# Kernel tuning notes

Measured on AMD Instinct MI355X. Metric: run time of the kernel, lower is better.

The kernel has to match this reference:

```python
import jax, jax.numpy as jnp
import numpy as np

# ---- constants mirroring the module config ----
NH = 64          # num_horizontal
NV = 8           # num_vertical (height slices)
GH = 51.2        # grid_size_h (meters)
GV = 8.0         # grid_size_v (meters)
HF, WF = 26, 88  # ground feature map spatial shape (grd_spatial_shape_cross)
IMG_H, IMG_W = 416.0, 1408.0  # kitti_grd_size (H, W)
C = 256          # embed_dim
HEADS = 8
P = 4            # num_points (num_levels = 1)
DH = C // HEADS
NU = NH // 2 + 1  # 33
LQ = NU * NH      # 2112 queries


def _grid3d():
    x_ = np.linspace(-GH / 2, 0, NU)
    y_ = np.linspace(-GH / 2, GH / 2, NH)
    z_ = np.linspace(-GV / 2, GV / 2, NV)
    gx, gy, gz = np.meshgrid(x_, y_, z_, indexing='ij')
    g = np.stack([gy, -gz, -gx], axis=-1).reshape(-1, 3).astype(np.float32)
    return jnp.asarray(g)  # (NU*NH*NV, 3)


def setup_inputs() -> dict:
    key = jax.random.key(0)
    ks = jax.random.split(key, 8)
    bs = 2
    query = jax.random.normal(ks[0], (bs, LQ, C), jnp.float32)
    value = jax.random.normal(ks[1], (bs, HF * WF, C), jnp.float32)
    K = jnp.array([[984.0, 0.0, 704.0], [0.0, 984.0, 208.0], [0.0, 0.0, 1.0]], jnp.float32)
    camera_k = jnp.broadcast_to(K, (bs, 3, 3))
    s = 1.0 / np.sqrt(C)
    Wv = jax.random.normal(ks[2], (C, C), jnp.float32) * s
    bv = jnp.zeros((C,), jnp.float32)
    Wo = jax.random.normal(ks[3], (C, HEADS * P * 2), jnp.float32) * 0.02
    bo = jax.random.normal(ks[4], (HEADS * P * 2,), jnp.float32) * 0.5
    Wa = jax.random.normal(ks[5], (C, HEADS * P), jnp.float32) * 0.02
    ba = jnp.zeros((HEADS * P,), jnp.float32)
    Wout = jax.random.normal(ks[6], (C, C), jnp.float32) * s
    bout = jnp.zeros((C,), jnp.float32)
    Wp = jax.random.normal(ks[7], (C, 1), jnp.float32) * s
    bp = jnp.zeros((1,), jnp.float32)
    return dict(query=query, value=value, camera_k=camera_k, Wv=Wv, bv=bv,
                Wo=Wo, bo=bo, Wa=Wa, ba=ba, Wout=Wout, bout=bout, Wp=Wp, bp=bp)


def _bilinear(val, x, y):
    # val: (bs, HF, WF, heads, dh); x, y: (bs, S, heads) pixel coords (align_corners=False, zero pad)
    bs, H_, W_, nh, _ = val.shape
    x0f = jnp.floor(x)
    y0f = jnp.floor(y)
    lx = x - x0f
    ly = y - y0f
    x0 = x0f.astype(jnp.int32)
    y0 = y0f.astype(jnp.int32)
    b_idx = jnp.arange(bs)[:, None, None]
    h_idx = jnp.arange(nh)[None, None, :]

    def corner(xi, yi, w):
        valid = (xi >= 0) & (xi < W_) & (yi >= 0) & (yi < H_)
        xc = jnp.clip(xi, 0, W_ - 1)
        yc = jnp.clip(yi, 0, H_ - 1)
        g = val[b_idx, yc, xc, h_idx]  # (bs, S, heads, dh)
        return g * (w * valid)[..., None]

    return (corner(x0, y0, (1 - lx) * (1 - ly))
            + corner(x0 + 1, y0, lx * (1 - ly))
            + corner(x0, y0 + 1, (1 - lx) * ly)
            + corner(x0 + 1, y0 + 1, lx * ly))


def reference(query, value, camera_k, Wv, bv, Wo, bo, Wa, ba, Wout, bout, Wp, bp):
    bs = query.shape[0]
    g = _grid3d()                                       # (N3, 3)
    proj = jnp.einsum('bij,nj->bin', camera_k, g)       # (bs, 3, N3)
    den = proj[:, 2]
    den = jnp.where(jnp.abs(den) < 1e-6, 1e-6, den)     # sanitize depth-0 points
    u = (proj[:, 0] / den / IMG_W).reshape(bs, NU, NH, NV)
    v = (proj[:, 1] / den / IMG_H).reshape(bs, NU, NH, NV)
    keep_index = ((u >= 0) & (u <= 1) & (v >= 0) & (v <= 1)).sum(-1).astype(bool)

    # --- MultiScaleDeformableAttention, vectorized over the NV height slices ---
    valp = (value @ Wv + bv).reshape(bs, HF, WF, HEADS, DH)
    off = (query @ Wo + bo).reshape(bs, LQ, HEADS, P, 2)
    attn = jax.nn.softmax((query @ Wa + ba).reshape(bs, LQ, HEADS, P), axis=-1)

    ref = jnp.stack([u, v], axis=-1).transpose(0, 3, 1, 2, 4).reshape(bs, NV, LQ, 2)
    norm = jnp.array([WF, HF], jnp.float32)            # offset_normalizer = (W, H)
    loc = ref[:, :, :, None, None, :] + off[:, None] / norm  # (bs, NV, LQ, heads, P, 2)
    # grid_sample align_corners=False: pixel = loc*size - 0.5
    px = jnp.clip(loc[..., 0] * WF - 0.5, -1e4, 1e4)
    py = jnp.clip(loc[..., 1] * HF - 0.5, -1e4, 1e4)
    px = px.transpose(0, 1, 2, 4, 3).reshape(bs, -1, HEADS)  # (bs, NV*LQ*P, heads)
    py = py.transpose(0, 1, 2, 4, 3).reshape(bs, -1, HEADS)
    sampled = _bilinear(valp, px, py).reshape(bs, NV, LQ, P, HEADS, DH)
    msda = jnp.einsum('bqhp,bvqphd->bvqhd', attn, sampled).reshape(bs, NV, LQ, C)
    grd_bev_v = msda @ Wout + bout + query[:, None]     # MSDA internal identity residual

    # --- softmax-weighted pooling over height ---
    grd_3d = grd_bev_v.reshape(bs, NV, NU, NH, C).transpose(0, 2, 3, 1, 4)  # (bs,NU,NH,NV,C)
    w = jax.nn.softmax(grd_3d @ Wp + bp, axis=3)        # (bs, NU, NH, NV, 1)
    max_height_index = jnp.argmax(w, axis=3)            # (bs, NU, NH, 1)
    grd_bev = (w * grd_3d).sum(3).reshape(bs, LQ, C) + query
    return grd_bev, max_height_index, keep_index
```

## Files before the change

### kernel.cpp

```cpp
#include <hip/hip_runtime.h>
#include <hip/hip_bf16.h>

constexpr int kNV = 8;
constexpr int kHF = 26;
constexpr int kWF = 88;
constexpr int kC  = 256;
constexpr int kP  = 4;
constexpr int kNU = 33;
constexpr int kNH = 64;
constexpr int kLQ = kNU * kNH;

typedef short short8 __attribute__((ext_vector_type(8)));
typedef float floatx4 __attribute__((ext_vector_type(4)));

__device__ __forceinline__ unsigned short f2bf(float x) {
  __hip_bfloat16 h = __float2bfloat16(x);
  unsigned short u;
  __builtin_memcpy(&u, &h, 2);
  return u;
}

template <bool VIRT>
__device__ __forceinline__ void gemm_body(
    const float* __restrict__ A, const float* __restrict__ B,
    const float* __restrict__ bias,
    const float* __restrict__ Wo, const float* __restrict__ Wa,
    const float* __restrict__ bo, const float* __restrict__ ba,
    float* __restrict__ out, int M, int N, int K, int bx, int by) {
  __shared__ float As[32][36];
  __shared__ float Bs[32][64];
  int tid = threadIdx.x;
  int tx = tid & 15, ty = tid >> 4;
  int row0 = by * 32, col0 = bx * 64;
  int ar = tid >> 3, ak = (tid & 7) * 4;
  int bc = (tid & 15) * 4, bk = tid >> 4;
  bool arow_ok = (row0 + ar) < M;
  const float* Ap = A + (size_t)(row0 + ar) * K + ak;
  int cb = col0 + bc;
  float acc[2][4] = {};
  for (int k0 = 0; k0 < K; k0 += 32) {
    float4 a4 = {0.f, 0.f, 0.f, 0.f};
    if (arow_ok) a4 = *reinterpret_cast<const float4*>(Ap + k0);
    float4 b0, b1;
    if (!VIRT) {
      b0 = *reinterpret_cast<const float4*>(&B[(size_t)(k0 + bk) * N + cb]);
      b1 = *reinterpret_cast<const float4*>(&B[(size_t)(k0 + bk + 16) * N + cb]);
    } else {
      if (cb < 64) {
        b0 = *reinterpret_cast<const float4*>(&Wo[(k0 + bk) * 64 + cb]);
        b1 = *reinterpret_cast<const float4*>(&Wo[(k0 + bk + 16) * 64 + cb]);
      } else if (cb < 96) {
        b0 = *reinterpret_cast<const float4*>(&Wa[(k0 + bk) * 32 + cb - 64]);
        b1 = *reinterpret_cast<const float4*>(&Wa[(k0 + bk + 16) * 32 + cb - 64]);
      } else {
        b0 = float4{0.f, 0.f, 0.f, 0.f};
        b1 = float4{0.f, 0.f, 0.f, 0.f};
      }
    }
    __syncthreads();
    *reinterpret_cast<float4*>(&As[ar][ak]) = a4;
    *reinterpret_cast<float4*>(&Bs[bk][bc]) = b0;
    *reinterpret_cast<float4*>(&Bs[bk + 16][bc]) = b1;
    __syncthreads();
#pragma unroll
    for (int kk = 0; kk < 32; ++kk) {
      float a0 = As[ty * 2][kk];
      float a1 = As[ty * 2 + 1][kk];
      float4 b4 = *reinterpret_cast<const float4*>(&Bs[kk][tx * 4]);
      acc[0][0] += a0 * b4.x; acc[0][1] += a0 * b4.y;
      acc[0][2] += a0 * b4.z; acc[0][3] += a0 * b4.w;
      acc[1][0] += a1 * b4.x; acc[1][1] += a1 * b4.y;
      acc[1][2] += a1 * b4.z; acc[1][3] += a1 * b4.w;
    }
  }
  int gc = col0 + tx * 4;
  float4 bi;
  if (!VIRT) {
    bi = *reinterpret_cast<const float4*>(&bias[gc]);
  } else if (gc < 64) {
    bi = *reinterpret_cast<const float4*>(&bo[gc]);
  } else if (gc < 96) {
    bi = *reinterpret_cast<const float4*>(&ba[gc - 64]);
  } else {
    bi = float4{0.f, 0.f, 0.f, 0.f};
  }
#pragma unroll
  for (int i = 0; i < 2; ++i) {
    int gr = row0 + ty * 2 + i;
    if (gr >= M) continue;
    float4 r;
    r.x = acc[i][0] + bi.x; r.y = acc[i][1] + bi.y;
    r.z = acc[i][2] + bi.z; r.w = acc[i][3] + bi.w;
    *reinterpret_cast<float4*>(&out[(size_t)gr * N + gc]) = r;
  }
}

__global__ __launch_bounds__(256) void k_front(
    const float* __restrict__ value, const float* __restrict__ Wv,
    const float* __restrict__ bv, float* __restrict__ valp,
    const float* __restrict__ query, float* __restrict__ qcat,
    const float* __restrict__ Wo, const float* __restrict__ Wa,
    const float* __restrict__ bo, const float* __restrict__ ba,
    const float* __restrict__ camk, float* __restrict__ uv,
    float* __restrict__ out_keep,
    const float* __restrict__ Wout, const float* __restrict__ Wp,
    float* __restrict__ WoutWp, unsigned short* __restrict__ WoutT,
    int bs, int MV, int MQ, int nValp, int nQ, int nGeomBlk) {
  int blk = blockIdx.x;
  int tid = threadIdx.x;
  if (blk < nValp) {
    gemm_body<false>(value, Wv, bv, nullptr, nullptr, nullptr, nullptr,
                     valp, MV, kC, kC, blk & 3, blk >> 2);
  } else if (blk < nValp + nQ) {
    int r = blk - nValp;
    gemm_body<true>(query, nullptr, nullptr, Wo, Wa, bo, ba,
                    qcat, MQ, 128, kC, r & 1, r >> 1);
  } else if (blk < nValp + nQ + nGeomBlk) {
    int t = (blk - nValp - nQ) * 256 + tid;
    if (t >= bs * kLQ) return;
    int b = t / kLQ;
    int ij = t - b * kLQ;
    int i = ij / kNH;
    int j = ij - i * kNH;
    const float* K = camk + b * 9;
    float g0 = (float)(-25.6 + (double)j * (51.2 / 63.0));
    float g2 = (float)(25.6 - (double)i * 0.8);
    bool any = false;
    float* dst = uv + (size_t)t * 16;
    for (int k = 0; k < kNV; ++k) {
      float g1 = (float)(4.0 - (double)k * (8.0 / 7.0));
      float p0 = K[0] * g0 + K[1] * g1 + K[2] * g2;
      float p1 = K[3] * g0 + K[4] * g1 + K[5] * g2;
      float p2 = K[6] * g0 + K[7] * g1 + K[8] * g2;
      float den = (fabsf(p2) < 1e-6f) ? 1e-6f : p2;
      float u = p0 / den / 1408.0f;
      float v = p1 / den / 416.0f;
      any = any || (u >= 0.f && u <= 1.f && v >= 0.f && v <= 1.f);
      dst[k * 2]     = u;
      dst[k * 2 + 1] = v;
    }
    out_keep[t] = any ? 1.f : 0.f;
  } else if (blk < nValp + nQ + nGeomBlk + 64) {
    int r = (blk - nValp - nQ - nGeomBlk) * 4 + (tid >> 6);
    int lane = tid & 63;
    const float* row = Wout + (size_t)r * kC;
    float s = 0.f;
#pragma unroll
    for (int j = lane; j < kC; j += 64) s += row[j] * Wp[j];
#pragma unroll
    for (int o = 32; o > 0; o >>= 1) s += __shfl_down(s, o, 64);
    if (lane == 0) WoutWp[r] = s;
  } else {
    int c = blk - nValp - nQ - nGeomBlk - 64;
    WoutT[(size_t)c * kC + tid] = f2bf(Wout[(size_t)tid * kC + c]);
  }
}

__global__ __launch_bounds__(256) void gemm_mfma(
    const unsigned short* __restrict__ Abf, const unsigned short* __restrict__ BT,
    const float* __restrict__ bias, const float* __restrict__ query,
    float* __restrict__ out, int M) {
  int gw = blockIdx.x * 4 + (threadIdx.x >> 6);
  int lane = threadIdx.x & 63;
  int tr = gw >> 4;
  int tc = gw & 15;
  int r0 = tr * 16, c0 = tc * 16;
  if (r0 >= M) return;
  int lrow = lane & 15;
  int kgrp = lane >> 4;
  const unsigned short* Ap = Abf + (size_t)(r0 + lrow) * kC + kgrp * 8;
  const unsigned short* Bp = BT  + (size_t)(c0 + lrow) * kC + kgrp * 8;
  floatx4 acc = {0.f, 0.f, 0.f, 0.f};
#pragma unroll
  for (int k0 = 0; k0 < kC; k0 += 32) {
    short8 a = *reinterpret_cast<const short8*>(Ap + k0);
    short8 b = *reinterpret_cast<const short8*>(Bp + k0);
    acc = __builtin_amdgcn_mfma_f32_16x16x32_bf16(a, b, acc, 0, 0, 0);
  }
  int col = c0 + lrow;
  float bi = bias[col];
#pragma unroll
  for (int r = 0; r < 4; ++r) {
    int row = r0 + kgrp * 4 + r;
    out[(size_t)row * kC + col] =
        acc[r] + bi + 2.0f * query[(size_t)row * kC + col];
  }
}

__global__ __launch_bounds__(256) void k_fused(
    const float* __restrict__ valp, const float* __restrict__ uv,
    const float* __restrict__ qcat, const float* __restrict__ WoutWp,
    unsigned short* __restrict__ msda_bf, float* __restrict__ out_mhi) {
  int bq = blockIdx.x;
  int b = bq / kLQ;
  int tid = threadIdx.x;
  int wp = tid >> 6;
  int lane = tid & 63;
  int h = lane >> 3;
  int dq = lane & 7;
  int ch = h * 32 + dq * 4;

  const float* qp = qcat + (size_t)bq * 128;

  float4 qa4 = *reinterpret_cast<const float4*>(qp + 64 + h * 4);
  float am = fmaxf(fmaxf(qa4.x, qa4.y), fmaxf(qa4.z, qa4.w));
  float e0 = expf(qa4.x - am), e1 = expf(qa4.y - am);
  float e2 = expf(qa4.z - am), e3 = expf(qa4.w - am);
  float ei = 1.f / (e0 + e1 + e2 + e3);
  float aw[4] = {e0 * ei, e1 * ei, e2 * ei, e3 * ei};

  float4 qo0 = *reinterpret_cast<const float4*>(qp + h * 8);
  float4 qo1 = *reinterpret_cast<const float4*>(qp + h * 8 + 4);
  float offx[4] = {qo0.x, qo0.z, qo1.x, qo1.z};
  float offy[4] = {qo0.y, qo0.w, qo1.y, qo1.w};

  float4 t4 = reinterpret_cast<const float4*>(uv + (size_t)bq * 16)[wp];
  float ub[2], vb[2];
  ub[0] = t4.x * 88.0f - 0.5f;
  vb[0] = t4.y * 26.0f - 0.5f;
  ub[1] = t4.z * 88.0f - 0.5f;
  vb[1] = t4.w * 26.0f - 0.5f;

  const float* vp = valp + (size_t)b * (kHF * kWF) * kC + ch;
  float4 w4 = *reinterpret_cast<const float4*>(WoutWp + ch);

  __shared__ float lgs[kNV];
  __shared__ float wks[kNV];
  __shared__ float4 part[3][64];

  float4 sv[2];
#pragma unroll
  for (int vv = 0; vv < 2; ++vv) {
    float4 s4 = {0.f, 0.f, 0.f, 0.f};
#pragma unroll
    for (int p = 0; p < kP; ++p) {
      float px = ub[vv] + offx[p];
      float py = vb[vv] + offy[p];
      px = fminf(fmaxf(px, -10000.f), 10000.f);
      py = fminf(fmaxf(py, -10000.f), 10000.f);
      if (px >= -1.f && px < 88.f && py >= -1.f && py < 26.f) {
        float x0f = floorf(px), y0f = floorf(py);
        float lx = px - x0f, ly = py - y0f;
        int x0 = (int)x0f, y0 = (int)y0f;
#pragma unroll
        for (int cy = 0; cy < 2; ++cy) {
#pragma unroll
          for (int cx = 0; cx < 2; ++cx) {
            int xi = x0 + cx, yi = y0 + cy;
            float w = (cx ? lx : 1.f - lx) * (cy ? ly : 1.f - ly) * aw[p];
            bool valid = (xi >= 0) && (xi < kWF) && (yi >= 0) && (yi < kHF);
            int xc = xi < 0 ? 0 : (xi > kWF - 1 ? kWF - 1 : xi);
            int yc = yi < 0 ? 0 : (yi > kHF - 1 ? kHF - 1 : yi);
            float4 g = *reinterpret_cast<const float4*>(vp + (yc * kWF + xc) * kC);
            float wv = valid ? w : 0.f;
            s4.x += wv * g.x; s4.y += wv * g.y; s4.z += wv * g.z; s4.w += wv * g.w;
          }
        }
      }
    }
    sv[vv] = s4;
    float lv = s4.x * w4.x + s4.y * w4.y + s4.z * w4.z + s4.w * w4.w;
#pragma unroll
    for (int o = 32; o > 0; o >>= 1) lv += __shfl_down(lv, o, 64);
    if (lane == 0) lgs[wp * 2 + vv] = lv;
  }
  __syncthreads();
  if (tid == 0) {
    float m = -1e30f; int ai = 0;
#pragma unroll
    for (int v = 0; v < kNV; ++v)
      if (lgs[v] > m) { m = lgs[v]; ai = v; }
    float ssum = 0.f;
    float ev[kNV];
#pragma unroll
    for (int v = 0; v < kNV; ++v) { ev[v] = expf(lgs[v] - m); ssum += ev[v]; }
    float invs = 1.f / ssum;
#pragma unroll
    for (int v = 0; v < kNV; ++v) wks[v] = ev[v] * invs;
    out_mhi[bq] = (float)ai;
  }
  __syncthreads();
  float4 acc = {0.f, 0.f, 0.f, 0.f};
#pragma unroll
  for (int vv = 0; vv < 2; ++vv) {
    float wv = wks[wp * 2 + vv];
    acc.x += wv * sv[vv].x; acc.y += wv * sv[vv].y;
    acc.z += wv * sv[vv].z; acc.w += wv * sv[vv].w;
  }
  if (wp > 0) part[wp - 1][lane] = acc;
  __syncthreads();
  if (wp == 0) {
#pragma unroll
    for (int i = 0; i < 3; ++i) {
      float4 pp = part[i][lane];
      acc.x += pp.x; acc.y += pp.y; acc.z += pp.z; acc.w += pp.w;
    }
    ushort4 pk;
    pk.x = f2bf(acc.x); pk.y = f2bf(acc.y);
    pk.z = f2bf(acc.z); pk.w = f2bf(acc.w);
    *reinterpret_cast<ushort4*>(msda_bf + (size_t)bq * kC + ch) = pk;
  }
}

extern "C" void kernel_launch(void* const* d_in, const int* in_sizes, int n_in,
                              void* d_out, int out_size, void* d_ws, size_t ws_size,
                              hipStream_t stream) {
  if (n_in < 13) return;
  const float* query = (const float*)d_in[0];
  const float* value = (const float*)d_in[1];
  const float* camk  = (const float*)d_in[2];
  const float* Wv    = (const float*)d_in[3];
  const float* bv    = (const float*)d_in[4];
  const float* Wo    = (const float*)d_in[5];
  const float* bo    = (const float*)d_in[6];
  const float* Wa    = (const float*)d_in[7];
  const float* ba    = (const float*)d_in[8];
  const float* Wout  = (const float*)d_in[9];
  const float* bout  = (const float*)d_in[10];
  const float* Wp    = (const float*)d_in[11];
  int bs = in_sizes[0] / (kLQ * kC);
  int MQ = bs * kLQ;
  int MV = bs * kHF * kWF;

  float* ws = (float*)d_ws;
  size_t o = 0;
  float* valp    = ws + o; o += (size_t)MV * kC;
  float* uv      = ws + o; o += (size_t)MQ * 16;
  float* qcat    = ws + o; o += (size_t)MQ * 128;
  unsigned short* msda_bf = (unsigned short*)(ws + o); o += (size_t)MQ * kC / 2;
  float* WoutWp  = ws + o; o += kC;
  unsigned short* WoutT = (unsigned short*)(ws + o); o += (size_t)kC * kC / 2;
  (void)ws_size; (void)out_size;

  float* outp = (float*)d_out;
  float* out_grd  = outp;
  float* out_mhi  = outp + (size_t)MQ * kC;
  float* out_keep = out_mhi + (size_t)MQ;

  int nGeomBlk = (MQ + 255) / 256;
  int yb0 = (MV + 31) / 32;
  int yb1 = (MQ + 31) / 32;
  int nValp = 4 * yb0;
  int nQ = 2 * yb1;
  k_front<<<nValp + nQ + nGeomBlk + 64 + 256, 256, 0, stream>>>(
      value, Wv, bv, valp, query, qcat, Wo, Wa, bo, ba,
      camk, uv, out_keep, Wout, Wp, WoutWp, WoutT,
      bs, MV, MQ, nValp, nQ, nGeomBlk);
  k_fused<<<MQ, 256, 0, stream>>>(valp, uv, qcat, WoutWp, msda_bf, out_mhi);
  gemm_mfma<<<MQ / 4, 256, 0, stream>>>(msda_bf, WoutT, bout, query, out_grd, MQ);
}
```

Measured before the change: 53.52 us.

## Use 512-thread blocks in fused sampling kernel, one wave per height slice

The fused deformable-sampling kernel now launches 512 threads per query, so each of the 8 wavefronts handles one height slice instead of each of 4 waves handling two. This exposes more memory-level parallelism for the scattered bilinear gathers and shortens each wave's serial chain of dependent loads. In exchange the block-level reduction grows from 3 to 7 partial buffers in shared memory. Larger blocks also duplicate the per-query softmax and offset setup across more waves and may reduce how many blocks fit per CU.

After: 55.54 us. 3.8% more time.

```diff
diff --git a/kernel.cpp b/kernel.cpp
--- a/kernel.cpp
+++ b/kernel.cpp
@@ -187,7 +187,7 @@
   }
 }
 
-__global__ __launch_bounds__(256) void k_fused(
+__global__ __launch_bounds__(512) void k_fused(
     const float* __restrict__ valp, const float* __restrict__ uv,
     const float* __restrict__ qcat, const float* __restrict__ WoutWp,
     unsigned short* __restrict__ msda_bf, float* __restrict__ out_mhi) {
@@ -214,56 +214,48 @@
   float offx[4] = {qo0.x, qo0.z, qo1.x, qo1.z};
   float offy[4] = {qo0.y, qo0.w, qo1.y, qo1.w};
 
-  float4 t4 = reinterpret_cast<const float4*>(uv + (size_t)bq * 16)[wp];
-  float ub[2], vb[2];
-  ub[0] = t4.x * 88.0f - 0.5f;
-  vb[0] = t4.y * 26.0f - 0.5f;
-  ub[1] = t4.z * 88.0f - 0.5f;
-  vb[1] = t4.w * 26.0f - 0.5f;
+  float4 t4 = reinterpret_cast<const float4*>(uv + (size_t)bq * 16)[wp >> 1];
+  float ub = (wp & 1) ? (t4.z * 88.0f - 0.5f) : (t4.x * 88.0f - 0.5f);
+  float vb = (wp & 1) ? (t4.w * 26.0f - 0.5f) : (t4.y * 26.0f - 0.5f);
 
   const float* vp = valp + (size_t)b * (kHF * kWF) * kC + ch;
   float4 w4 = *reinterpret_cast<const float4*>(WoutWp + ch);
 
   __shared__ float lgs[kNV];
   __shared__ float wks[kNV];
-  __shared__ float4 part[3][64];
-
-  float4 sv[2];
-#pragma unroll
-  for (int vv = 0; vv < 2; ++vv) {
-    float4 s4 = {0.f, 0.f, 0.f, 0.f};
-#pragma unroll
-    for (int p = 0; p < kP; ++p) {
-      float px = ub[vv] + offx[p];
-      float py = vb[vv] + offy[p];
-      px = fminf(fmaxf(px, -10000.f), 10000.f);
-      py = fminf(fmaxf(py, -10000.f), 10000.f);
-      if (px >= -1.f && px < 88.f && py >= -1.f && py < 26.f) {
-        float x0f = floorf(px), y0f = floorf(py);
-        float lx = px - x0f, ly = py - y0f;
-        int x0 = (int)x0f, y0 = (int)y0f;
-#pragma unroll
-        for (int cy = 0; cy < 2; ++cy) {
-#pragma unroll
-          for (int cx = 0; cx < 2; ++cx) {
-            int xi = x0 + cx, yi = y0 + cy;
-            float w = (cx ? lx : 1.f - lx) * (cy ? ly : 1.f - ly) * aw[p];
-            bool valid = (xi >= 0) && (xi < kWF) && (yi >= 0) && (yi < kHF);
-            int xc = xi < 0 ? 0 : (xi > kWF - 1 ? kWF - 1 : xi);
-            int yc = yi < 0 ? 0 : (yi > kHF - 1 ? kHF - 1 : yi);
-            float4 g = *reinterpret_cast<const float4*>(vp + (yc * kWF + xc) * kC);
-            float wv = valid ? w : 0.f;
-            s4.x += wv * g.x; s4.y += wv * g.y; s4.z += wv * g.z; s4.w += wv * g.w;
-          }
+  __shared__ float4 part[7][64];
+
+  float4 s4 = {0.f, 0.f, 0.f, 0.f};
+#pragma unroll
+  for (int p = 0; p < kP; ++p) {
+    float px = ub + offx[p];
+    float py = vb + offy[p];
+    px = fminf(fmaxf(px, -10000.f), 10000.f);
+    py = fminf(fmaxf(py, -10000.f), 10000.f);
+    if (px >= -1.f && px < 88.f && py >= -1.f && py < 26.f) {
+      float x0f = floorf(px), y0f = floorf(py);
+      float lx = px - x0f, ly = py - y0f;
+      int x0 = (int)x0f, y0 = (int)y0f;
+#pragma unroll
+      for (int cy = 0; cy < 2; ++cy) {
+#pragma unroll
+        for (int cx = 0; cx < 2; ++cx) {
+          int xi = x0 + cx, yi = y0 + cy;
+          float w = (cx ? lx : 1.f - lx) * (cy ? ly : 1.f - ly) * aw[p];
+          bool valid = (xi >= 0) && (xi < kWF) && (yi >= 0) && (yi < kHF);
+          int xc = xi < 0 ? 0 : (xi > kWF - 1 ? kWF - 1 : xi);
+          int yc = yi < 0 ? 0 : (yi > kHF - 1 ? kHF - 1 : yi);
+          float4 g = *reinterpret_cast<const float4*>(vp + (yc * kWF + xc) * kC);
+          float wv = valid ? w : 0.f;
+          s4.x += wv * g.x; s4.y += wv * g.y; s4.z += wv * g.z; s4.w += wv * g.w;
         }
       }
     }
-    sv[vv] = s4;
-    float lv = s4.x * w4.x + s4.y * w4.y + s4.z * w4.z + s4.w * w4.w;
-#pragma unroll
-    for (int o = 32; o > 0; o >>= 1) lv += __shfl_down(lv, o, 64);
-    if (lane == 0) lgs[wp * 2 + vv] = lv;
-  }
+  }
+  float lv = s4.x * w4.x + s4.y * w4.y + s4.z * w4.z + s4.w * w4.w;
+#pragma unroll
+  for (int o = 32; o > 0; o >>= 1) lv += __shfl_down(lv, o, 64);
+  if (lane == 0) lgs[wp] = lv;
   __syncthreads();
   if (tid == 0) {
     float m = -1e30f; int ai = 0;
@@ -280,18 +272,14 @@
     out_mhi[bq] = (float)ai;
   }
   __syncthreads();
-  float4 acc = {0.f, 0.f, 0.f, 0.f};
-#pragma unroll
-  for (int vv = 0; vv < 2; ++vv) {
-    float wv = wks[wp * 2 + vv];
-    acc.x += wv * sv[vv].x; acc.y += wv * sv[vv].y;
-    acc.z += wv * sv[vv].z; acc.w += wv * sv[vv].w;
-  }
+  float wv = wks[wp];
+  float4 acc;
+  acc.x = wv * s4.x; acc.y = wv * s4.y; acc.z = wv * s4.z; acc.w = wv * s4.w;
   if (wp > 0) part[wp - 1][lane] = acc;
   __syncthreads();
   if (wp == 0) {
 #pragma unroll
-    for (int i = 0; i < 3; ++i) {
+    for (int i = 0; i < 7; ++i) {
       float4 pp = part[i][lane];
       acc.x += pp.x; acc.y += pp.y; acc.z += pp.z; acc.w += pp.w;
     }
@@ -346,6 +334,6 @@
       value, Wv, bv, valp, query, qcat, Wo, Wa, bo, ba,
       camk, uv, out_keep, Wout, Wp, WoutWp, WoutT,
       bs, MV, MQ, nValp, nQ, nGeomBlk);
-  k_fused<<<MQ, 256, 0, stream>>>(valp, uv, qcat, WoutWp, msda_bf, out_mhi);
+  k_fused<<<MQ, 512, 0, stream>>>(valp, uv, qcat, WoutWp, msda_bf, out_mhi);
   gemm_mfma<<<MQ / 4, 256, 0, stream>>>(msda_bf, WoutT, bout, query, out_grd, MQ);
 }
```
